# Kernel tuning notes

Hardware: AMD Instinct MI355X
Metric: run time of the kernel (lower is better)

## Reference

```python
import jax, jax.numpy as jnp
import numpy as np

B, S, D, H = 4, 2048, 1024, 16
DH = D // H  # 64


def setup_inputs() -> dict:
    key = jax.random.key(0)
    ks = jax.random.split(key, 8)
    scale = 1.0 / np.sqrt(D)  # xavier-ish init for square linears
    return {
        "query": jax.random.normal(ks[0], (B, S, D), jnp.float32),
        "key": jax.random.normal(ks[1], (B, S, D), jnp.float32),
        "value": jax.random.normal(ks[2], (B, S, D), jnp.float32),
        "mask": jax.random.randint(ks[3], (B, 1, 1, S), 0, 2).astype(jnp.bool_),
        "Wq": jax.random.normal(ks[4], (D, D), jnp.float32) * scale,
        "Wk": jax.random.normal(ks[5], (D, D), jnp.float32) * scale,
        "Wv": jax.random.normal(ks[6], (D, D), jnp.float32) * scale,
        "Wo": jax.random.normal(ks[7], (D, D), jnp.float32) * scale,
    }


def _split_heads(x):
    # (B, S, D) -> (B, H, S, DH)
    b, s, _ = x.shape
    return x.reshape(b, s, H, DH).transpose(0, 2, 1, 3)


def reference(query, key, value, mask, Wq, Wk, Wv, Wo):
    # Linear projections (torch Linear: x @ W.T, no bias)
    q = _split_heads(query @ Wq.T)   # (B, H, S, DH)
    k = _split_heads(key @ Wk.T)     # (B, H, S, DH)
    v = _split_heads(value @ Wv.T)   # (B, H, S, DH)

    # Scaled dot-product attention: softmax(QK^T / sqrt(d_head)) V
    scores = jnp.einsum("bhqd,bhkd->bhqk", q, k) / np.sqrt(DH).astype(np.float32)
    # masked_fill_(mask, -1e9): True entries are masked out
    scores = jnp.where(mask, jnp.float32(-1e9), scores)
    attn = jax.nn.softmax(scores, axis=-1)
    # dropout: identity at inference (eval mode)
    ctx = jnp.einsum("bhqk,bhkd->bhqd", attn, v)  # (B, H, S, DH)

    # Merge heads and apply output projection
    ctx = ctx.transpose(0, 2, 1, 3).reshape(query.shape[0], -1, H * DH)
    return ctx @ Wo.T
```

## Files before the change

kernel.cpp:

```cpp
#include <hip/hip_runtime.h>


#define BB 4
#define SS 2048
#define DD 1024
#define HH 16
#define DH 64

typedef __bf16 bf16x8 __attribute__((ext_vector_type(8)));
typedef float floatx4 __attribute__((ext_vector_type(4)));
typedef unsigned short ushortx8 __attribute__((ext_vector_type(8)));
typedef unsigned short ushortx4 __attribute__((ext_vector_type(4)));
typedef unsigned short ushort_t;

__device__ __forceinline__ unsigned short f2bf(float f) {
    unsigned u = __builtin_bit_cast(unsigned, f);
    u += 0x7FFFu + ((u >> 16) & 1u);
    return (unsigned short)(u >> 16);
}

__device__ __forceinline__ bf16x8 ldb(const ushort_t* p) {
    return __builtin_bit_cast(bf16x8, *(const ushortx8*)p);
}

__device__ __forceinline__ void dma16(const ushort_t* g, ushort_t* l) {
    __builtin_amdgcn_global_load_lds(
        (const __attribute__((address_space(1))) unsigned int*)g,
        (__attribute__((address_space(3))) unsigned int*)l, 16, 0, 0);
}

__device__ __forceinline__ floatx4 mfma32(bf16x8 a, bf16x8 b, floatx4 c) {
    return __builtin_amdgcn_mfma_f32_16x16x32_bf16(a, b, c, 0, 0, 0);
}

__device__ __forceinline__ floatx4 fzero() {
    floatx4 z = {0.f, 0.f, 0.f, 0.f};
    return z;
}

__global__ void cvt_all(const float* __restrict__ q, const float* __restrict__ k,
                        const float* __restrict__ v, const float* __restrict__ wq,
                        const float* __restrict__ wk, const float* __restrict__ wv,
                        const float* __restrict__ wo,
                        ushort_t* __restrict__ oq, ushort_t* __restrict__ ok,
                        ushort_t* __restrict__ ov, ushort_t* __restrict__ owqkv,
                        ushort_t* __restrict__ owo) {
    const int bid = blockIdx.x;
    const float* in; ushort_t* out; int rel;
    if (bid < 8192)        { in = q;  out = oq;            rel = bid; }
    else if (bid < 16384)  { in = k;  out = ok;            rel = bid - 8192; }
    else if (bid < 24576)  { in = v;  out = ov;            rel = bid - 16384; }
    else if (bid < 25600)  { in = wq; out = owqkv;         rel = bid - 24576; }
    else if (bid < 26624)  { in = wk; out = owqkv + 1048576; rel = bid - 25600; }
    else if (bid < 27648)  { in = wv; out = owqkv + 2097152; rel = bid - 26624; }
    else                   { in = wo; out = owo;           rel = bid - 27648; }
    int i = rel * 1024 + threadIdx.x * 4;
    float4 f = *(const float4*)&in[i];
    ushortx4 o;
    o[0] = f2bf(f.x); o[1] = f2bf(f.y); o[2] = f2bf(f.z); o[3] = f2bf(f.w);
    *(ushortx4*)&out[i] = o;
}

__device__ __forceinline__ void gemm_core(
    const ushort_t* __restrict__ Ab, const ushort_t* __restrict__ Bb,
    floatx4 acc[4][4], ushort_t (*As)[128][32], ushort_t (*Bs)[128][32], int tid)
{
    const int wv = tid >> 6, lane = tid & 63;
    const int quad = lane >> 4, lid = lane & 15;
    const int wm = wv & 1, wn = wv >> 1;
    const int r0 = lane >> 2, c0 = (lane & 3) * 8;

#pragma unroll
    for (int i = 0; i < 4; ++i)
#pragma unroll
        for (int j = 0; j < 4; ++j) acc[i][j] = fzero();

#pragma unroll
    for (int s = 0; s < 2; ++s) {
        int seg = wv * 2 + s;
        dma16(&Ab[(size_t)(seg * 16 + r0) * DD + c0], &As[0][seg * 16][0]);
        dma16(&Bb[(size_t)(seg * 16 + r0) * DD + c0], &Bs[0][seg * 16][0]);
    }
    __syncthreads();

    int cur = 0;
    for (int k0 = 0; k0 < DD; k0 += 32) {
        int nxt = cur ^ 1;
        if (k0 + 32 < DD) {
#pragma unroll
            for (int s = 0; s < 2; ++s) {
                int seg = wv * 2 + s;
                dma16(&Ab[(size_t)(seg * 16 + r0) * DD + k0 + 32 + c0], &As[nxt][seg * 16][0]);
                dma16(&Bb[(size_t)(seg * 16 + r0) * DD + k0 + 32 + c0], &Bs[nxt][seg * 16][0]);
            }
        }
        bf16x8 af[4], bfr[4];
#pragma unroll
        for (int mt = 0; mt < 4; ++mt) af[mt] = ldb(&As[cur][wm * 64 + mt * 16 + lid][quad * 8]);
#pragma unroll
        for (int nt = 0; nt < 4; ++nt) bfr[nt] = ldb(&Bs[cur][wn * 64 + nt * 16 + lid][quad * 8]);
#pragma unroll
        for (int mt = 0; mt < 4; ++mt)
#pragma unroll
            for (int nt = 0; nt < 4; ++nt)
                acc[mt][nt] = mfma32(af[mt], bfr[nt], acc[mt][nt]);
        __syncthreads();
        cur = nxt;
    }
}

__global__ __launch_bounds__(256) void gemm_qkv(
    const ushort_t* __restrict__ Qa, const ushort_t* __restrict__ Ka,
    const ushort_t* __restrict__ Va, const ushort_t* __restrict__ Wqkv,
    const int* __restrict__ maskg,
    ushort_t* __restrict__ Qp, ushort_t* __restrict__ Kp, ushort_t* __restrict__ Vtp)
{
    __shared__ ushort_t As[2][128][32];
    __shared__ ushort_t Bs[2][128][32];
    ushort_t (*Ts)[16][72] = reinterpret_cast<ushort_t (*)[16][72]>(&As[0][0][0]);

    const int tid = threadIdx.x;
    const int f = blockIdx.x;
    const int logical = (f & 7) * 192 + (f >> 3);
    const int by = logical / 24;
    const int bxx = logical % 24;
    const int which = bxx >> 3;
    const int m0 = by * 128;
    const int n0 = bxx * 128;
    const ushort_t* Ab = (which == 0 ? Qa : which == 1 ? Ka : Va) + (size_t)m0 * DD;
    const ushort_t* Bb = Wqkv + (size_t)n0 * DD;

    floatx4 acc[4][4];
    gemm_core(Ab, Bb, acc, As, Bs, tid);

    const int wv = tid >> 6, lane = tid & 63;
    const int quad = lane >> 4, lid = lane & 15;
    const int wm = wv & 1, wn = wv >> 1;
    const int b = m0 >> 11;
    const int sbase = (m0 & 2047) + wm * 64;
    const int nl0 = n0 - which * 1024 + wn * 64;
    const int sl = lane >> 2, cl = (lane & 3) * 16;
    const int* maskb = maskg + b * SS;

    if (which == 2) {
#pragma unroll
        for (int nt = 0; nt < 4; ++nt) {
#pragma unroll
            for (int mt = 0; mt < 4; ++mt) {
                int sp = sbase + mt * 16 + quad * 4;
                int4 mv = *(const int4*)&maskb[sp];
                ushortx4 o;
                o[0] = mv.x ? (ushort_t)0 : f2bf(acc[mt][nt][0]);
                o[1] = mv.y ? (ushort_t)0 : f2bf(acc[mt][nt][1]);
                o[2] = mv.z ? (ushort_t)0 : f2bf(acc[mt][nt][2]);
                o[3] = mv.w ? (ushort_t)0 : f2bf(acc[mt][nt][3]);
                *(ushortx4*)&Ts[wv][lid][mt * 16 + quad * 4] = o;
            }
            ushortx8 w0 = *(const ushortx8*)&Ts[wv][sl][cl];
            ushortx8 w1 = *(const ushortx8*)&Ts[wv][sl][cl + 8];
            int nl = nl0 + nt * 16 + sl;
            int h = nl >> 6, dh = nl & 63;
            size_t base = (((size_t)b * HH + h) * DH + dh) * SS + sbase + cl;
            *(ushortx8*)&Vtp[base] = w0;
            *(ushortx8*)&Vtp[base + 8] = w1;
        }
    } else {
        ushort_t* P = which ? Kp : Qp;
        const float scl = which ? 1.0f : 0.125f * 1.4426950408889634f;
        const int h = nl0 >> 6;
#pragma unroll
        for (int mt = 0; mt < 4; ++mt) {
            int mvr[4] = {0, 0, 0, 0};
            if (which) {
                int4 mv = *(const int4*)&maskb[sbase + mt * 16 + quad * 4];
                mvr[0] = mv.x; mvr[1] = mv.y; mvr[2] = mv.z; mvr[3] = mv.w;
            }
#pragma unroll
            for (int nt = 0; nt < 4; ++nt)
#pragma unroll
                for (int r = 0; r < 4; ++r)
                    Ts[wv][quad * 4 + r][nt * 16 + lid] =
                        mvr[r] ? (ushort_t)0 : f2bf(acc[mt][nt][r] * scl);
            ushortx8 w0 = *(const ushortx8*)&Ts[wv][sl][cl];
            ushortx8 w1 = *(const ushortx8*)&Ts[wv][sl][cl + 8];
            int s = sbase + mt * 16 + sl;
            size_t base = (((size_t)b * HH + h) * SS + s) * DH + (nl0 & 63) + cl;
            *(ushortx8*)&P[base] = w0;
            *(ushortx8*)&P[base + 8] = w1;
        }
    }
}

__global__ __launch_bounds__(256) void gemm_o(
    const ushort_t* __restrict__ Cx, const ushort_t* __restrict__ Wo,
    float* __restrict__ Out)
{
    __shared__ ushort_t As[2][128][32];
    __shared__ ushort_t Bs[2][128][32];
    const int tid = threadIdx.x;
    const int f = blockIdx.x;
    const int logical = (f & 7) * 64 + (f >> 3);
    const int by = logical >> 3, bx = logical & 7;
    const int m0 = by * 128;
    const int n0 = bx * 128;

    floatx4 acc[4][4];
    gemm_core(Cx + (size_t)m0 * DD, Wo + (size_t)n0 * DD, acc, As, Bs, tid);

    const int wv = tid >> 6, lane = tid & 63;
    const int quad = lane >> 4, lid = lane & 15;
    const int wm = wv & 1, wn = wv >> 1;
#pragma unroll
    for (int mt = 0; mt < 4; ++mt)
#pragma unroll
        for (int nt = 0; nt < 4; ++nt)
#pragma unroll
            for (int r = 0; r < 4; ++r) {
                int m = m0 + wm * 64 + mt * 16 + quad * 4 + r;
                int n = n0 + wn * 64 + nt * 16 + lid;
                Out[(size_t)m * DD + n] = acc[mt][nt][r];
            }
}

__global__ __launch_bounds__(256) void attn_kernel(
    const ushort_t* __restrict__ Qg, const ushort_t* __restrict__ Kg,
    const ushort_t* __restrict__ Vtg, const int* __restrict__ maskg,
    ushort_t* __restrict__ Ctx)
{
    __shared__ ushort_t Ks[2][64 * 64];
    __shared__ ushort_t Vts[2][64 * 64];

    const int flat = blockIdx.x;
    const int xcd = flat & 7;
    const int slot = flat >> 3;
    const int bh = xcd * 8 + (slot >> 4);
    const int qc = slot & 15;
    const int b = bh >> 4, h = bh & 15;
    const int tid = threadIdx.x;
    const int wv = tid >> 6, lane = tid & 63;
    const int quad = lane >> 4, lid = lane & 15;

    const ushort_t* Qb = Qg + (size_t)bh * SS * DH;
    const ushort_t* Kb = Kg + (size_t)bh * SS * DH;
    const ushort_t* Vtb = Vtg + (size_t)bh * DH * SS;
    const int* maskb = maskg + b * SS;

    int nm = 0;
    {
        const int4* m4 = (const int4*)maskb;
#pragma unroll
        for (int i = 0; i < 8; ++i) {
            int4 m = m4[lane + i * 64];
            nm += m.x + m.y + m.z + m.w;
        }
#pragma unroll
        for (int off = 32; off; off >>= 1) nm += __shfl_xor(nm, off);
    }
    const float nmf = (float)nm;

    const int qbase = qc * 128 + wv * 32;

    bf16x8 qf[2][2];
#pragma unroll
    for (int g = 0; g < 2; ++g) {
        const int row = qbase + g * 16 + lid;
        qf[g][0] = ldb(&Qb[(size_t)row * DH + quad * 8]);
        qf[g][1] = ldb(&Qb[(size_t)row * DH + 32 + quad * 8]);
    }

    ushortx8 ov;
#pragma unroll
    for (int i = 0; i < 8; ++i) ov[i] = (ushort_t)0x3F80;
    const bf16x8 ones = __builtin_bit_cast(bf16x8, ov);

    int offK[2], offV[2];
#pragma unroll
    for (int s = 0; s < 2; ++s) {
        int idx = wv * 128 + s * 64 + lane;
        int row = idx >> 3;
        int c16 = idx & 7;
        int p = (row & 35) | ((row & 12) << 1) | ((row & 16) >> 2);
        int colu = (c16 ^ (row & 7)) << 3;
        offK[s] = p * DH + colu;
        offV[s] = row * SS + colu;
    }

    floatx4 Oacc[2][4];
    floatx4 Osum[2];
#pragma unroll
    for (int g = 0; g < 2; ++g) {
        Osum[g] = fzero();
#pragma unroll
        for (int i = 0; i < 4; ++i) Oacc[g][i] = fzero();
    }

    const int swz = (lid & 7) << 3;

    dma16(Kb + offK[0], &Ks[0][(wv * 2 + 0) * 512]);
    dma16(Kb + offK[1], &Ks[0][(wv * 2 + 1) * 512]);
    dma16(Vtb + offV[0], &Vts[0][(wv * 2 + 0) * 512]);
    dma16(Vtb + offV[1], &Vts[0][(wv * 2 + 1) * 512]);
    __syncthreads();

    const ushort_t* Kc = Kb + 64 * DH;
    const ushort_t* Vc = Vtb + 64;
    int cur = 0;

    for (int kc = 0; kc < SS / 64; ++kc) {
        int nxt = cur ^ 1;
        if (kc + 1 < SS / 64) {
            dma16(Kc + offK[0], &Ks[nxt][(wv * 2 + 0) * 512]);
            dma16(Kc + offK[1], &Ks[nxt][(wv * 2 + 1) * 512]);
            dma16(Vc + offV[0], &Vts[nxt][(wv * 2 + 0) * 512]);
            dma16(Vc + offV[1], &Vts[nxt][(wv * 2 + 1) * 512]);
            Kc += 64 * DH;
            Vc += 64;
        }

#pragma unroll
        for (int kk = 0; kk < 2; ++kk) {
            floatx4 sA[2], sB[2];
            __builtin_amdgcn_s_setprio(1);
#pragma unroll
            for (int m2 = 0; m2 < 2; ++m2) {
                const int mt = kk * 2 + m2;
                const int rb = (mt * 16 + lid) * 64;
                bf16x8 kf0 = ldb(&Ks[cur][rb + ((quad * 8) ^ swz)]);
                bf16x8 kf1 = ldb(&Ks[cur][rb + ((32 + quad * 8) ^ swz)]);
                sA[m2] = mfma32(kf1, qf[0][1], mfma32(kf0, qf[0][0], fzero()));
                sB[m2] = mfma32(kf1, qf[1][1], mfma32(kf0, qf[1][0], fzero()));
            }
            __builtin_amdgcn_s_setprio(0);
            bf16x8 pa, pb;
#pragma unroll
            for (int r = 0; r < 4; ++r) {
                pa[r]     = (__bf16)__builtin_amdgcn_exp2f(sA[0][r]);
                pa[r + 4] = (__bf16)__builtin_amdgcn_exp2f(sA[1][r]);
                pb[r]     = (__bf16)__builtin_amdgcn_exp2f(sB[0][r]);
                pb[r + 4] = (__bf16)__builtin_amdgcn_exp2f(sB[1][r]);
            }
            __builtin_amdgcn_s_setprio(1);
            Osum[0] = mfma32(pa, ones, Osum[0]);
            Osum[1] = mfma32(pb, ones, Osum[1]);
#pragma unroll
            for (int nt = 0; nt < 4; ++nt) {
                bf16x8 vb = ldb(&Vts[cur][(nt * 16 + lid) * 64 + ((kk * 32 + quad * 8) ^ swz)]);
                Oacc[0][nt] = mfma32(pa, vb, Oacc[0][nt]);
                Oacc[1][nt] = mfma32(pb, vb, Oacc[1][nt]);
            }
            __builtin_amdgcn_s_setprio(0);
        }
        __syncthreads();
        cur = nxt;
    }

#pragma unroll
    for (int g = 0; g < 2; ++g) {
        float inv[4];
#pragma unroll
        for (int r = 0; r < 4; ++r) inv[r] = 1.0f / (Osum[g][r] - nmf);
#pragma unroll
        for (int nt = 0; nt < 4; ++nt) {
#pragma unroll
            for (int r = 0; r < 4; ++r) {
                int s = qbase + g * 16 + quad * 4 + r;
                int dh = nt * 16 + lid;
                Ctx[(((size_t)b * SS + s) * HH + h) * DH + dh] = f2bf(Oacc[g][nt][r] * inv[r]);
            }
        }
    }
}

extern "C" void kernel_launch(void* const* d_in, const int* in_sizes, int n_in,
                              void* d_out, int out_size, void* d_ws, size_t ws_size,
                              hipStream_t stream) {
    const float* q  = (const float*)d_in[0];
    const float* k  = (const float*)d_in[1];
    const float* v  = (const float*)d_in[2];
    const int*   mask = (const int*)d_in[3];
    const float* Wq = (const float*)d_in[4];
    const float* Wk = (const float*)d_in[5];
    const float* Wv = (const float*)d_in[6];
    const float* Wo = (const float*)d_in[7];
    float* out = (float*)d_out;

    char* ws = (char*)d_ws;
    const size_t MB = 1024 * 1024;
    ushort_t* Qin  = (ushort_t*)(ws + 0 * MB);
    ushort_t* Kin  = (ushort_t*)(ws + 16 * MB);
    ushort_t* Vin  = (ushort_t*)(ws + 32 * MB);
    ushort_t* Qp   = (ushort_t*)(ws + 48 * MB);
    ushort_t* Kp   = (ushort_t*)(ws + 64 * MB);
    ushort_t* Vtp  = (ushort_t*)(ws + 80 * MB);
    ushort_t* Wqkv = (ushort_t*)(ws + 96 * MB);
    ushort_t* Wob  = (ushort_t*)(ws + 102 * MB);
    ushort_t* Cx   = Qin;

    cvt_all<<<dim3(28672), 256, 0, stream>>>(q, k, v, Wq, Wk, Wv, Wo,
                                             Qin, Kin, Vin, Wqkv, Wob);

    gemm_qkv<<<dim3(1536), 256, 0, stream>>>(Qin, Kin, Vin, Wqkv, mask, Qp, Kp, Vtp);
    attn_kernel<<<dim3(1024), 256, 0, stream>>>(Qp, Kp, Vtp, mask, Cx);
    gemm_o<<<dim3(512), 256, 0, stream>>>(Cx, Wob, out);
}
```

Baseline: 328.0 us.

## Triple-buffer GEMM LDS tiles with vmcnt waits and one barrier per step

```diff
diff --git a/kernel.cpp b/kernel.cpp
--- a/kernel.cpp
+++ b/kernel.cpp
@@ -61,6 +61,19 @@
     *(ushortx4*)&out[i] = o;
 }
 
+__device__ __forceinline__ void stage_tile(
+    const ushort_t* __restrict__ Ab, const ushort_t* __restrict__ Bb,
+    ushort_t (*As)[128][32], ushort_t (*Bs)[128][32],
+    int buf, int k0, int wv, int r0, int c0)
+{
+#pragma unroll
+    for (int s = 0; s < 2; ++s) {
+        int seg = wv * 2 + s;
+        dma16(&Ab[(size_t)(seg * 16 + r0) * DD + k0 + c0], &As[buf][seg * 16][0]);
+        dma16(&Bb[(size_t)(seg * 16 + r0) * DD + k0 + c0], &Bs[buf][seg * 16][0]);
+    }
+}
+
 __device__ __forceinline__ void gemm_core(
     const ushort_t* __restrict__ Ab, const ushort_t* __restrict__ Bb,
     floatx4 acc[4][4], ushort_t (*As)[128][32], ushort_t (*Bs)[128][32], int tid)
@@ -75,38 +88,33 @@
 #pragma unroll
         for (int j = 0; j < 4; ++j) acc[i][j] = fzero();
 
-#pragma unroll
-    for (int s = 0; s < 2; ++s) {
-        int seg = wv * 2 + s;
-        dma16(&Ab[(size_t)(seg * 16 + r0) * DD + c0], &As[0][seg * 16][0]);
-        dma16(&Bb[(size_t)(seg * 16 + r0) * DD + c0], &Bs[0][seg * 16][0]);
-    }
-    __syncthreads();
-
-    int cur = 0;
-    for (int k0 = 0; k0 < DD; k0 += 32) {
-        int nxt = cur ^ 1;
-        if (k0 + 32 < DD) {
-#pragma unroll
-            for (int s = 0; s < 2; ++s) {
-                int seg = wv * 2 + s;
-                dma16(&Ab[(size_t)(seg * 16 + r0) * DD + k0 + 32 + c0], &As[nxt][seg * 16][0]);
-                dma16(&Bb[(size_t)(seg * 16 + r0) * DD + k0 + 32 + c0], &Bs[nxt][seg * 16][0]);
-            }
+    stage_tile(Ab, Bb, As, Bs, 0, 0, wv, r0, c0);
+    stage_tile(Ab, Bb, As, Bs, 1, 32, wv, r0, c0);
+
+    int bc = 0;
+    int bs2 = 2;
+    for (int t = 0; t < 32; ++t) {
+        if (t < 31) { asm volatile("s_waitcnt vmcnt(4)" ::: "memory"); }
+        else        { asm volatile("s_waitcnt vmcnt(0)" ::: "memory"); }
+        asm volatile("s_barrier" ::: "memory");
+        if (t < 30) {
+            stage_tile(Ab, Bb, As, Bs, bs2, (t + 2) * 32, wv, r0, c0);
+            bs2 = (bs2 == 2) ? 0 : bs2 + 1;
         }
         bf16x8 af[4], bfr[4];
 #pragma unroll
-        for (int mt = 0; mt < 4; ++mt) af[mt] = ldb(&As[cur][wm * 64 + mt * 16 + lid][quad * 8]);
-#pragma unroll
-        for (int nt = 0; nt < 4; ++nt) bfr[nt] = ldb(&Bs[cur][wn * 64 + nt * 16 + lid][quad * 8]);
+        for (int mt = 0; mt < 4; ++mt) af[mt] = ldb(&As[bc][wm * 64 + mt * 16 + lid][quad * 8]);
+#pragma unroll
+        for (int nt = 0; nt < 4; ++nt) bfr[nt] = ldb(&Bs[bc][wn * 64 + nt * 16 + lid][quad * 8]);
 #pragma unroll
         for (int mt = 0; mt < 4; ++mt)
 #pragma unroll
             for (int nt = 0; nt < 4; ++nt)
                 acc[mt][nt] = mfma32(af[mt], bfr[nt], acc[mt][nt]);
-        __syncthreads();
-        cur = nxt;
-    }
+        asm volatile("s_waitcnt lgkmcnt(0)" ::: "memory");
+        bc = (bc == 2) ? 0 : bc + 1;
+    }
+    __syncthreads();
 }
 
 __global__ __launch_bounds__(256) void gemm_qkv(
@@ -115,8 +123,8 @@
     const int* __restrict__ maskg,
     ushort_t* __restrict__ Qp, ushort_t* __restrict__ Kp, ushort_t* __restrict__ Vtp)
 {
-    __shared__ ushort_t As[2][128][32];
-    __shared__ ushort_t Bs[2][128][32];
+    __shared__ ushort_t As[3][128][32];
+    __shared__ ushort_t Bs[3][128][32];
     ushort_t (*Ts)[16][72] = reinterpret_cast<ushort_t (*)[16][72]>(&As[0][0][0]);
 
     const int tid = threadIdx.x;
@@ -195,8 +203,8 @@
     const ushort_t* __restrict__ Cx, const ushort_t* __restrict__ Wo,
     float* __restrict__ Out)
 {
-    __shared__ ushort_t As[2][128][32];
-    __shared__ ushort_t Bs[2][128][32];
+    __shared__ ushort_t As[3][128][32];
+    __shared__ ushort_t Bs[3][128][32];
     const int tid = threadIdx.x;
     const int f = blockIdx.x;
     const int logical = (f & 7) * 64 + (f >> 3);
```

Measured after the change: 347.6 us. 1.06x slower.
